# Performance work log

Measured on AMD Instinct MI355X. Metric: run time of the kernel, lower is better.

The kernel has to match this reference:

```python
import jax, jax.numpy as jnp
import numpy as np

N, E = 100000, 1600000
IN, T, H, C = 56, 16, 4, 16
HID, OUT = 64, 64
NEG_SLOPE = 0.2   # PyG GATConv default negative_slope
LN_EPS = 1e-5


def setup_inputs() -> dict:
    key = jax.random.key(0)
    k = jax.random.split(key, 12)
    g = lambda kk, shape: jax.random.normal(kk, shape, jnp.float32) * 0.1
    return {
        "x": jax.random.normal(k[0], (N, IN), jnp.float32),
        "temporal_features": jax.random.normal(k[1], (N, 1), jnp.float32),
        "edge_index": jax.random.randint(k[2], (2, E), 0, N, dtype=jnp.int32),
        "Wt": g(k[3], (1, T)), "bt": jnp.zeros((T,), jnp.float32),
        "W1": g(k[4], (IN + T, H * C)), "a_src1": g(k[5], (H, C)), "a_dst1": g(k[6], (H, C)),
        "b1": jnp.zeros((HID,), jnp.float32),
        "g1": jnp.ones((HID,), jnp.float32), "beta1": jnp.zeros((HID,), jnp.float32),
        "W2": g(k[7], (HID, H * C)), "a_src2": g(k[8], (H, C)), "a_dst2": g(k[9], (H, C)),
        "b2": jnp.zeros((OUT,), jnp.float32),
        "g2": jnp.ones((OUT,), jnp.float32), "beta2": jnp.zeros((OUT,), jnp.float32),
        "Wp1": g(k[10], (OUT, HID)), "bp1": jnp.zeros((HID,), jnp.float32),
        "Wp2": g(k[11], (HID, OUT)), "bp2": jnp.zeros((OUT,), jnp.float32),
    }


def _layer_norm(x, gamma, beta):
    mu = jnp.mean(x, -1, keepdims=True)
    var = jnp.var(x, -1, keepdims=True)
    return (x - mu) * jax.lax.rsqrt(var + LN_EPS) * gamma + beta


def _gat(x, src, dst, W, a_src, a_dst, bias, n):
    # linear transform per head (lin has no bias in PyG GATConv)
    h = (x @ W).reshape(n, H, C)                       # [N,H,C]
    s = jnp.einsum('nhc,hc->nh', h, a_src)             # att_src . h, per node
    d = jnp.einsum('nhc,hc->nh', h, a_dst)             # att_dst . h, per node
    e = jax.nn.leaky_relu(s[src] + d[dst], NEG_SLOPE)  # [Etot,H] per-edge logits
    # segment softmax over destination node (PyG softmax with +1e-16 denom)
    m = jax.ops.segment_max(e, dst, num_segments=n)
    e = jnp.exp(e - m[dst])
    z = jax.ops.segment_sum(e, dst, num_segments=n)
    alpha = e / (z[dst] + 1e-16)
    out = jax.ops.segment_sum(alpha[:, :, None] * h[src], dst, num_segments=n)
    return out.reshape(n, H * C) + bias


def reference(x, temporal_features, edge_index, Wt, bt, W1, a_src1, a_dst1, b1, g1, beta1,
              W2, a_src2, a_dst2, b2, g2, beta2, Wp1, bp1, Wp2, bp2):
    n = x.shape[0]
    t = jax.nn.relu(temporal_features @ Wt + bt)       # temporal encoder (dropout=identity, eval)
    xc = jnp.concatenate([x, t], axis=1)               # [N, 72]
    # add self-loops (PyG GATConv default add_self_loops=True)
    loop = jnp.arange(n, dtype=edge_index.dtype)
    src = jnp.concatenate([edge_index[0], loop])
    dst = jnp.concatenate([edge_index[1], loop])
    x1 = jax.nn.relu(_layer_norm(_gat(xc, src, dst, W1, a_src1, a_dst1, b1, n), g1, beta1))
    x2 = jax.nn.relu(_layer_norm(_gat(x1, src, dst, W2, a_src2, a_dst2, b2, n), g2, beta2))
    ge = jnp.mean(x2, axis=0)                          # batch=None -> global mean over nodes
    ge = jax.nn.relu(ge @ Wp1 + bp1) @ Wp2 + bp2       # global_pool MLP, then squeeze(0)
    return x2, ge
```

## Files before the change

### kernel.cpp

```cpp
#include <hip/hip_runtime.h>
#include <hip/hip_bf16.h>

#define NN    100000
#define EE    1600000
#define INF   56
#define TFEAT 16
#define K1    72

#define BUCKET_BITS 10
#define BUCKET_NODES (1 << BUCKET_BITS)
#define NB ((NN + BUCKET_NODES - 1) >> BUCKET_BITS)
#define BUCKET_CAP 20480
#define S1_EDGES 1024

__device__ __forceinline__ void fatomic_add(float* p, float v) {
    __hip_atomic_fetch_add(p, v, __ATOMIC_RELAXED, __HIP_MEMORY_SCOPE_AGENT);
}

__device__ __forceinline__ float lrelu(float v) { return v > 0.f ? v : 0.2f * v; }
__device__ __forceinline__ float bf2f(__hip_bfloat16 b) { return __bfloat162float(b); }
__device__ __forceinline__ float bfu2f(unsigned short u) {
    return __uint_as_float((unsigned)u << 16);
}
__device__ __forceinline__ unsigned short f2bfu(float f) {
    __hip_bfloat16 b = __float2bfloat16(f);
    return *reinterpret_cast<unsigned short*>(&b);
}

template <int K, bool TEMPORAL, bool IN_BF16>
__global__ void __launch_bounds__(256) feat_kernel(
    const void* __restrict__ xin_, const float* __restrict__ temp,
    const float* __restrict__ Wt, const float* __restrict__ bt,
    const float* __restrict__ W, const float* __restrict__ asrc,
    const float* __restrict__ adst,
    __hip_bfloat16* __restrict__ h, float* __restrict__ s, float* __restrict__ d)
{
    constexpr int NPB = 64;
    constexpr int WROW = 76;
    __shared__ float4 Wl4[K * 16];
    __shared__ __align__(16) float xc[NPB * WROW];
    const int tid = threadIdx.x;
    const int n0 = blockIdx.x * NPB;

    for (int i = tid; i < K * 16; i += 256)
        Wl4[i] = *(const float4*)&W[(i >> 4) * 64 + (i & 15) * 4];

    if (TEMPORAL) {
        const float* xin = (const float*)xin_;
        for (int i = tid; i < NPB * INF; i += 256) {
            int n = i / INF, k = i - n * INF;
            int gn = n0 + n;
            xc[n * WROW + k] = (gn < NN) ? xin[gn * INF + k] : 0.f;
        }
        for (int i = tid; i < NPB * TFEAT; i += 256) {
            int n = i >> 4, j = i & 15;
            int gn = n0 + n;
            float tv = (gn < NN) ? temp[gn] * Wt[j] + bt[j] : 0.f;
            xc[n * WROW + INF + j] = tv > 0.f ? tv : 0.f;
        }
    } else {
        const ushort4* xv4 = (const ushort4*)xin_;
        for (int i = tid; i < NPB * 16; i += 256) {
            int n = i >> 4, q = i & 15;
            int gn = n0 + n;
            float4 f = {0.f, 0.f, 0.f, 0.f};
            if (gn < NN) {
                ushort4 u = xv4[gn * 16 + q];
                f.x = bfu2f(u.x); f.y = bfu2f(u.y); f.z = bfu2f(u.z); f.w = bfu2f(u.w);
            }
            *(float4*)&xc[n * WROW + q * 4] = f;
        }
    }
    __syncthreads();

    const int w = tid >> 6, lane = tid & 63;
    const int li = lane & 15, gg = lane >> 4;
    const int nb = w * 16 + gg * 4;

    float4 a0 = {0,0,0,0}, a1 = {0,0,0,0}, a2 = {0,0,0,0}, a3 = {0,0,0,0};
    const float4* xr0 = (const float4*)&xc[(nb + 0) * WROW];
    const float4* xr1 = (const float4*)&xc[(nb + 1) * WROW];
    const float4* xr2 = (const float4*)&xc[(nb + 2) * WROW];
    const float4* xr3 = (const float4*)&xc[(nb + 3) * WROW];

#define FMA4(A, XV) \
    A.x += XV.x * w0.x + XV.y * w1.x + XV.z * w2.x + XV.w * w3.x; \
    A.y += XV.x * w0.y + XV.y * w1.y + XV.z * w2.y + XV.w * w3.y; \
    A.z += XV.x * w0.z + XV.y * w1.z + XV.z * w2.z + XV.w * w3.z; \
    A.w += XV.x * w0.w + XV.y * w1.w + XV.z * w2.w + XV.w * w3.w;

#pragma unroll
    for (int k4 = 0; k4 < K / 4; k4++) {
        float4 w0 = Wl4[(4 * k4 + 0) * 16 + li];
        float4 w1 = Wl4[(4 * k4 + 1) * 16 + li];
        float4 w2 = Wl4[(4 * k4 + 2) * 16 + li];
        float4 w3 = Wl4[(4 * k4 + 3) * 16 + li];
        float4 x0 = xr0[k4], x1 = xr1[k4], x2 = xr2[k4], x3 = xr3[k4];
        FMA4(a0, x0) FMA4(a1, x1) FMA4(a2, x2) FMA4(a3, x3)
    }
#undef FMA4

    const int head = li >> 2;
    const float4 as4 = *(const float4*)&asrc[li * 4];
    const float4 ad4 = *(const float4*)&adst[li * 4];
    float vs[4], vd[4];
    float4* ap[4] = {&a0, &a1, &a2, &a3};
#pragma unroll
    for (int j = 0; j < 4; j++) {
        float4 a = *ap[j];
        vs[j] = a.x * as4.x + a.y * as4.y + a.z * as4.z + a.w * as4.w;
        vd[j] = a.x * ad4.x + a.y * ad4.y + a.z * ad4.z + a.w * ad4.w;
        vs[j] += __shfl_xor(vs[j], 1); vs[j] += __shfl_xor(vs[j], 2);
        vd[j] += __shfl_xor(vd[j], 1); vd[j] += __shfl_xor(vd[j], 2);
    }

    ushort4* hv4 = (ushort4*)h;
#pragma unroll
    for (int j = 0; j < 4; j++) {
        int gn = n0 + nb + j;
        if (gn < NN) {
            float4 a = *ap[j];
            ushort4 st = { f2bfu(a.x), f2bfu(a.y), f2bfu(a.z), f2bfu(a.w) };
            hv4[gn * 16 + li] = st;
            if ((li & 3) == 0) { s[gn * 4 + head] = vs[j]; d[gn * 4 + head] = vd[j]; }
        }
    }
}

__global__ void __launch_bounds__(256) csr_s1_kernel(
    const int* __restrict__ esrc, const int* __restrict__ edst,
    int* __restrict__ bucketCnt, int* __restrict__ ebuf)
{
    __shared__ int hist[NB];
    __shared__ int base[NB];
    __shared__ int loff[NB];
    const int tid = threadIdx.x;
    const int e0 = blockIdx.x * S1_EDGES;

    for (int i = tid; i < NB; i += 256) { hist[i] = 0; loff[i] = 0; }
    __syncthreads();

    int val[4], bk[4];
#pragma unroll
    for (int t = 0; t < 4; t++) {
        int e = e0 + t * 256 + tid;
        if (e < EE) {
            int sn = esrc[e], dn = edst[e];
            int b = dn >> BUCKET_BITS;
            bk[t] = b;
            val[t] = ((dn & (BUCKET_NODES - 1)) << 17) | sn;
            atomicAdd(&hist[b], 1);
        } else bk[t] = -1;
    }
    __syncthreads();
    for (int i = tid; i < NB; i += 256)
        base[i] = hist[i] ? atomicAdd(&bucketCnt[i], hist[i]) : 0;
    __syncthreads();
#pragma unroll
    for (int t = 0; t < 4; t++) {
        if (bk[t] >= 0) {
            int pos = atomicAdd(&loff[bk[t]], 1);
            ebuf[bk[t] * BUCKET_CAP + base[bk[t]] + pos] = val[t];
        }
    }
}

__global__ void __launch_bounds__(256) csr_s2_kernel(
    const int* __restrict__ bucketCnt, const int* __restrict__ ebuf,
    int* __restrict__ deg, int* __restrict__ rowptr, int* __restrict__ csr_src)
{
    __shared__ int hist2[BUCKET_NODES];
    __shared__ int wsum[4];
    __shared__ int partial[256];
    const int b = blockIdx.x;
    const int tid = threadIdx.x;
    const int cnt = bucketCnt[b];
    const int nb0 = b << BUCKET_BITS;
    const int nnodes = min(BUCKET_NODES, NN - nb0);
    const int* seg = ebuf + b * BUCKET_CAP;

    partial[tid] = (tid < b) ? bucketCnt[tid] : 0;
    __syncthreads();
    for (int o = 128; o; o >>= 1) {
        if (tid < o) partial[tid] += partial[tid + o];
        __syncthreads();
    }
    const int cbase = partial[0];
    __syncthreads();

    for (int i = tid; i < BUCKET_NODES; i += 256) hist2[i] = 0;
    __syncthreads();
    for (int e = tid; e < cnt; e += 256) atomicAdd(&hist2[seg[e] >> 17], 1);
    __syncthreads();

    const int i0 = tid * 4;
    int h0 = hist2[i0], h1 = hist2[i0 + 1], h2 = hist2[i0 + 2], h3 = hist2[i0 + 3];
    int local = h0 + h1 + h2 + h3;
    int lane = tid & 63, wid = tid >> 6;
    int inc = local;
    for (int o = 1; o < 64; o <<= 1) {
        int u = __shfl_up(inc, o);
        if (lane >= o) inc += u;
    }
    if (lane == 63) wsum[wid] = inc;
    __syncthreads();
    int wbase = 0;
    for (int w = 0; w < wid; w++) wbase += wsum[w];
    int ebase = wbase + inc - local;
    __syncthreads();

    if (i0 < nnodes)     { deg[nb0 + i0]     = h0; rowptr[nb0 + i0]     = cbase + ebase; }
    if (i0 + 1 < nnodes) { deg[nb0 + i0 + 1] = h1; rowptr[nb0 + i0 + 1] = cbase + ebase + h0; }
    if (i0 + 2 < nnodes) { deg[nb0 + i0 + 2] = h2; rowptr[nb0 + i0 + 2] = cbase + ebase + h0 + h1; }
    if (i0 + 3 < nnodes) { deg[nb0 + i0 + 3] = h3; rowptr[nb0 + i0 + 3] = cbase + ebase + h0 + h1 + h2; }
    hist2[i0]     = ebase;
    hist2[i0 + 1] = ebase + h0;
    hist2[i0 + 2] = ebase + h0 + h1;
    hist2[i0 + 3] = ebase + h0 + h1 + h2;
    __syncthreads();

    for (int e = tid; e < cnt; e += 256) {
        int v = seg[e];
        int pos = atomicAdd(&hist2[v >> 17], 1);
        csr_src[cbase + pos] = v & 0x1FFFF;
    }
}

template <bool OUT_BF16>
__global__ void __launch_bounds__(256) agg_ln_kernel(
    const int* __restrict__ csr_src, const int* __restrict__ rowptr, const int* __restrict__ deg,
    const float* __restrict__ s, const float* __restrict__ d, const __hip_bfloat16* __restrict__ h,
    const float* __restrict__ bias, const float* __restrict__ gamma, const float* __restrict__ beta,
    void* __restrict__ out_)
{
    const int tid = threadIdx.x;
    const int wid = tid >> 6, lane = tid & 63;
    const int g = lane >> 4;
    const int li = lane & 15;
    const int head = li >> 2;
    const int c0 = li * 4;
    const int n = blockIdx.x * 16 + wid * 4 + g;

    const ushort4* hv4 = (const ushort4*)h;

    const float dv = d[n * 4 + head];
    float a0, a1, a2, a3, z;
    {
        float w = __expf(lrelu(s[n * 4 + head] + dv));
        ushort4 hv = hv4[n * 16 + li];
        a0 = w * bfu2f(hv.x); a1 = w * bfu2f(hv.y);
        a2 = w * bfu2f(hv.z); a3 = w * bfu2f(hv.w);
        z = w;
    }
    int j = rowptr[n];
    const int jend = j + deg[n];
    for (; j + 2 <= jend; j += 2) {
        int s0 = csr_src[j], s1 = csr_src[j + 1];
        float w0 = __expf(lrelu(s[s0 * 4 + head] + dv));
        float w1 = __expf(lrelu(s[s1 * 4 + head] + dv));
        ushort4 h0 = hv4[s0 * 16 + li];
        ushort4 h1 = hv4[s1 * 16 + li];
        a0 += w0 * bfu2f(h0.x) + w1 * bfu2f(h1.x);
        a1 += w0 * bfu2f(h0.y) + w1 * bfu2f(h1.y);
        a2 += w0 * bfu2f(h0.z) + w1 * bfu2f(h1.z);
        a3 += w0 * bfu2f(h0.w) + w1 * bfu2f(h1.w);
        z += w0 + w1;
    }
    if (j < jend) {
        int s0 = csr_src[j];
        float w0 = __expf(lrelu(s[s0 * 4 + head] + dv));
        ushort4 h0 = hv4[s0 * 16 + li];
        a0 += w0 * bfu2f(h0.x); a1 += w0 * bfu2f(h0.y);
        a2 += w0 * bfu2f(h0.z); a3 += w0 * bfu2f(h0.w);
        z += w0;
    }

    const float rz = 1.f / (z + 1e-16f);
    const float4 bv = *(const float4*)&bias[c0];
    float v0 = a0 * rz + bv.x, v1 = a1 * rz + bv.y;
    float v2 = a2 * rz + bv.z, v3 = a3 * rz + bv.w;

    float sum = (v0 + v1) + (v2 + v3);
    float sq  = (v0 * v0 + v1 * v1) + (v2 * v2 + v3 * v3);
#pragma unroll
    for (int o = 8; o; o >>= 1) { sum += __shfl_xor(sum, o); sq += __shfl_xor(sq, o); }
    float mu = sum * (1.f / 64.f);
    float var = sq * (1.f / 64.f) - mu * mu;
    float rs = rsqrtf(var + 1e-5f);
    const float4 gv = *(const float4*)&gamma[c0];
    const float4 bev = *(const float4*)&beta[c0];
    float y0 = (v0 - mu) * rs * gv.x + bev.x; y0 = y0 > 0.f ? y0 : 0.f;
    float y1 = (v1 - mu) * rs * gv.y + bev.y; y1 = y1 > 0.f ? y1 : 0.f;
    float y2 = (v2 - mu) * rs * gv.z + bev.z; y2 = y2 > 0.f ? y2 : 0.f;
    float y3 = (v3 - mu) * rs * gv.w + bev.w; y3 = y3 > 0.f ? y3 : 0.f;

    if (OUT_BF16) {
        ushort4 st = { f2bfu(y0), f2bfu(y1), f2bfu(y2), f2bfu(y3) };
        ((ushort4*)out_)[n * 16 + li] = st;
    } else {
        float4 st = { y0, y1, y2, y3 };
        ((float4*)out_)[n * 16 + li] = st;
    }
}

__global__ void __launch_bounds__(256) mean_kernel(const float* __restrict__ xin, float* __restrict__ meanacc) {
    __shared__ float sd[256];
    const int wid = threadIdx.x >> 6, c = threadIdx.x & 63;
    float csum = 0.f;
    for (int grp = blockIdx.x; grp < NN / 4; grp += 512) {
        int n = grp * 4 + wid;
        csum += xin[n * 64 + c];
    }
    sd[threadIdx.x] = csum;
    __syncthreads();
    if (threadIdx.x < 64) {
        fatomic_add(&meanacc[threadIdx.x],
                    sd[threadIdx.x] + sd[64 + threadIdx.x] + sd[128 + threadIdx.x] + sd[192 + threadIdx.x]);
    }
}

__global__ void __launch_bounds__(64) mlp_kernel(
    const float* __restrict__ meanacc,
    const float* __restrict__ Wp1, const float* __restrict__ bp1,
    const float* __restrict__ Wp2, const float* __restrict__ bp2,
    float* __restrict__ out)
{
    __shared__ float mean[64], hid[64];
    int t = threadIdx.x;
    mean[t] = meanacc[t] * (1.f / (float)NN);
    __syncthreads();
    float acc = bp1[t];
#pragma unroll
    for (int i = 0; i < 64; i++) acc += mean[i] * Wp1[i * 64 + t];
    hid[t] = acc > 0.f ? acc : 0.f;
    __syncthreads();
    float o = bp2[t];
#pragma unroll
    for (int i = 0; i < 64; i++) o += hid[i] * Wp2[i * 64 + t];
    out[NN * 64 + t] = o;
}

extern "C" void kernel_launch(void* const* d_in, const int* in_sizes, int n_in,
                              void* d_out, int out_size, void* d_ws, size_t ws_size,
                              hipStream_t stream) {
    const float* x    = (const float*)d_in[0];
    const float* temp = (const float*)d_in[1];
    const int*   ei   = (const int*)d_in[2];
    const float* Wt   = (const float*)d_in[3];
    const float* bt   = (const float*)d_in[4];
    const float* W1   = (const float*)d_in[5];
    const float* as1  = (const float*)d_in[6];
    const float* ad1  = (const float*)d_in[7];
    const float* b1   = (const float*)d_in[8];
    const float* g1   = (const float*)d_in[9];
    const float* be1  = (const float*)d_in[10];
    const float* W2   = (const float*)d_in[11];
    const float* as2  = (const float*)d_in[12];
    const float* ad2  = (const float*)d_in[13];
    const float* b2   = (const float*)d_in[14];
    const float* g2   = (const float*)d_in[15];
    const float* be2  = (const float*)d_in[16];
    const float* Wp1  = (const float*)d_in[17];
    const float* bp1  = (const float*)d_in[18];
    const float* Wp2  = (const float*)d_in[19];
    const float* bp2  = (const float*)d_in[20];

    float* out = (float*)d_out;

    char* w = (char*)d_ws;
    __hip_bfloat16* hb   = (__hip_bfloat16*)w;   w += (size_t)NN * 64 * 2;
    __hip_bfloat16* x1b  = (__hip_bfloat16*)w;   w += (size_t)NN * 64 * 2;
    float* sbuf    = (float*)w;                  w += (size_t)NN * 4 * 4;
    float* dbuf    = (float*)w;                  w += (size_t)NN * 4 * 4;
    float* meanacc = (float*)w;                  w += 256;
    int* bucketCnt = (int*)w;                    w += 512;
    int* deg       = (int*)w;                    w += (size_t)NN * 4;
    int* rowptr    = (int*)w;                    w += (size_t)NN * 4;
    int* csr_src   = (int*)w;                    w += (size_t)EE * 4;
    int* ebuf      = (int*)w;                    w += (size_t)NB * BUCKET_CAP * 4;

    const int* esrc = ei;
    const int* edst = ei + EE;

    hipMemsetAsync(bucketCnt, 0, 512, stream);
    hipMemsetAsync(meanacc, 0, 256, stream);

    csr_s1_kernel<<<(EE + S1_EDGES - 1) / S1_EDGES, 256, 0, stream>>>(esrc, edst, bucketCnt, ebuf);
    csr_s2_kernel<<<NB, 256, 0, stream>>>(bucketCnt, ebuf, deg, rowptr, csr_src);

    const int fgrid = (NN + 63) / 64;

    feat_kernel<K1, true, false><<<fgrid, 256, 0, stream>>>(x, temp, Wt, bt, W1, as1, ad1, hb, sbuf, dbuf);
    agg_ln_kernel<true><<<NN / 16, 256, 0, stream>>>(csr_src, rowptr, deg, sbuf, dbuf, hb, b1, g1, be1, x1b);

    feat_kernel<64, false, true><<<fgrid, 256, 0, stream>>>(x1b, nullptr, nullptr, nullptr, W2, as2, ad2, hb, sbuf, dbuf);
    agg_ln_kernel<false><<<NN / 16, 256, 0, stream>>>(csr_src, rowptr, deg, sbuf, dbuf, hb, b2, g2, be2, out);

    mean_kernel<<<512, 256, 0, stream>>>(out, meanacc);
    mlp_kernel<<<1, 64, 0, stream>>>(meanacc, Wp1, bp1, Wp2, bp2, out);
}
```

Baseline: 369.4 us.

## Degree-sort nodes, widen aggregation lanes, fold exp scaling, fuse global mean

```diff
diff --git a/kernel.cpp b/kernel.cpp
--- a/kernel.cpp
+++ b/kernel.cpp
@@ -12,13 +12,12 @@
 #define NB ((NN + BUCKET_NODES - 1) >> BUCKET_BITS)
 #define BUCKET_CAP 20480
 #define S1_EDGES 1024
+#define LOG2E 1.44269504f
 
 __device__ __forceinline__ void fatomic_add(float* p, float v) {
     __hip_atomic_fetch_add(p, v, __ATOMIC_RELAXED, __HIP_MEMORY_SCOPE_AGENT);
 }
 
-__device__ __forceinline__ float lrelu(float v) { return v > 0.f ? v : 0.2f * v; }
-__device__ __forceinline__ float bf2f(__hip_bfloat16 b) { return __bfloat162float(b); }
 __device__ __forceinline__ float bfu2f(unsigned short u) {
     return __uint_as_float((unsigned)u << 16);
 }
@@ -26,6 +25,9 @@
     __hip_bfloat16 b = __float2bfloat16(f);
     return *reinterpret_cast<unsigned short*>(&b);
 }
+__device__ __forceinline__ float blo(unsigned u) { return __uint_as_float(u << 16); }
+__device__ __forceinline__ float bhi(unsigned u) { return __uint_as_float(u & 0xFFFF0000u); }
+__device__ __forceinline__ float ew(float t) { return exp2f(fmaxf(t, 0.2f * t)); }
 
 template <int K, bool TEMPORAL, bool IN_BF16>
 __global__ void __launch_bounds__(256) feat_kernel(
@@ -122,7 +124,10 @@
             float4 a = *ap[j];
             ushort4 st = { f2bfu(a.x), f2bfu(a.y), f2bfu(a.z), f2bfu(a.w) };
             hv4[gn * 16 + li] = st;
-            if ((li & 3) == 0) { s[gn * 4 + head] = vs[j]; d[gn * 4 + head] = vd[j]; }
+            if ((li & 3) == 0) {
+                s[gn * 4 + head] = vs[j] * LOG2E;
+                d[gn * 4 + head] = vd[j] * LOG2E;
+            }
         }
     }
 }
@@ -167,11 +172,14 @@
 
 __global__ void __launch_bounds__(256) csr_s2_kernel(
     const int* __restrict__ bucketCnt, const int* __restrict__ ebuf,
-    int* __restrict__ deg, int* __restrict__ rowptr, int* __restrict__ csr_src)
+    int* __restrict__ deg, int* __restrict__ rowptr, int* __restrict__ csr_src,
+    int* __restrict__ perm)
 {
     __shared__ int hist2[BUCKET_NODES];
     __shared__ int wsum[4];
     __shared__ int partial[256];
+    __shared__ int dhist[64];
+    __shared__ int dcur[64];
     const int b = blockIdx.x;
     const int tid = threadIdx.x;
     const int cnt = bucketCnt[b];
@@ -224,110 +232,165 @@
         int pos = atomicAdd(&hist2[v >> 17], 1);
         csr_src[cbase + pos] = v & 0x1FFFF;
     }
+
+    if (tid < 64) { dhist[tid] = 0; }
+    __syncthreads();
+    int dkey[4] = { -1, -1, -1, -1 };
+    int dv_[4] = { h0, h1, h2, h3 };
+#pragma unroll
+    for (int jj = 0; jj < 4; jj++) {
+        if (i0 + jj < nnodes) {
+            dkey[jj] = min(dv_[jj], 63);
+            atomicAdd(&dhist[dkey[jj]], 1);
+        }
+    }
+    __syncthreads();
+    if (tid < 64) {
+        int v = dhist[tid];
+        int ic = v;
+        for (int o = 1; o < 64; o <<= 1) {
+            int u = __shfl_up(ic, o);
+            if (tid >= o) ic += u;
+        }
+        dcur[tid] = ic - v;
+    }
+    __syncthreads();
+#pragma unroll
+    for (int jj = 0; jj < 4; jj++) {
+        if (dkey[jj] >= 0) {
+            int pos = atomicAdd(&dcur[dkey[jj]], 1);
+            perm[nb0 + pos] = nb0 + i0 + jj;
+        }
+    }
 }
 
 template <bool OUT_BF16>
 __global__ void __launch_bounds__(256) agg_ln_kernel(
+    const int* __restrict__ perm,
     const int* __restrict__ csr_src, const int* __restrict__ rowptr, const int* __restrict__ deg,
     const float* __restrict__ s, const float* __restrict__ d, const __hip_bfloat16* __restrict__ h,
     const float* __restrict__ bias, const float* __restrict__ gamma, const float* __restrict__ beta,
-    void* __restrict__ out_)
+    void* __restrict__ out_, float* __restrict__ meanslots)
 {
+    __shared__ float sd[32 * 65];
     const int tid = threadIdx.x;
     const int wid = tid >> 6, lane = tid & 63;
-    const int g = lane >> 4;
-    const int li = lane & 15;
-    const int head = li >> 2;
-    const int c0 = li * 4;
-    const int n = blockIdx.x * 16 + wid * 4 + g;
-
-    const ushort4* hv4 = (const ushort4*)h;
-
-    const float dv = d[n * 4 + head];
-    float a0, a1, a2, a3, z;
+    const int g = lane >> 3;
+    const int li = lane & 7;
+    const int head = li >> 1;
+    const int n = blockIdx.x * 32 + wid * 8 + g;
+    const int p = perm[n];
+
+    const uint4* hv4 = (const uint4*)h;
+
+    const float dv = d[p * 4 + head];
+    float a0, a1, a2, a3, a4, a5, a6, a7, z;
     {
-        float w = __expf(lrelu(s[n * 4 + head] + dv));
-        ushort4 hv = hv4[n * 16 + li];
-        a0 = w * bfu2f(hv.x); a1 = w * bfu2f(hv.y);
-        a2 = w * bfu2f(hv.z); a3 = w * bfu2f(hv.w);
+        float w = ew(s[p * 4 + head] + dv);
+        uint4 u = hv4[p * 8 + li];
+        a0 = w * blo(u.x); a1 = w * bhi(u.x);
+        a2 = w * blo(u.y); a3 = w * bhi(u.y);
+        a4 = w * blo(u.z); a5 = w * bhi(u.z);
+        a6 = w * blo(u.w); a7 = w * bhi(u.w);
         z = w;
     }
-    int j = rowptr[n];
-    const int jend = j + deg[n];
+    int j = rowptr[p];
+    const int jend = j + deg[p];
     for (; j + 2 <= jend; j += 2) {
         int s0 = csr_src[j], s1 = csr_src[j + 1];
-        float w0 = __expf(lrelu(s[s0 * 4 + head] + dv));
-        float w1 = __expf(lrelu(s[s1 * 4 + head] + dv));
-        ushort4 h0 = hv4[s0 * 16 + li];
-        ushort4 h1 = hv4[s1 * 16 + li];
-        a0 += w0 * bfu2f(h0.x) + w1 * bfu2f(h1.x);
-        a1 += w0 * bfu2f(h0.y) + w1 * bfu2f(h1.y);
-        a2 += w0 * bfu2f(h0.z) + w1 * bfu2f(h1.z);
-        a3 += w0 * bfu2f(h0.w) + w1 * bfu2f(h1.w);
+        float w0 = ew(s[s0 * 4 + head] + dv);
+        float w1 = ew(s[s1 * 4 + head] + dv);
+        uint4 u0 = hv4[s0 * 8 + li];
+        uint4 u1 = hv4[s1 * 8 + li];
+        a0 += w0 * blo(u0.x) + w1 * blo(u1.x);
+        a1 += w0 * bhi(u0.x) + w1 * bhi(u1.x);
+        a2 += w0 * blo(u0.y) + w1 * blo(u1.y);
+        a3 += w0 * bhi(u0.y) + w1 * bhi(u1.y);
+        a4 += w0 * blo(u0.z) + w1 * blo(u1.z);
+        a5 += w0 * bhi(u0.z) + w1 * bhi(u1.z);
+        a6 += w0 * blo(u0.w) + w1 * blo(u1.w);
+        a7 += w0 * bhi(u0.w) + w1 * bhi(u1.w);
         z += w0 + w1;
     }
     if (j < jend) {
         int s0 = csr_src[j];
-        float w0 = __expf(lrelu(s[s0 * 4 + head] + dv));
-        ushort4 h0 = hv4[s0 * 16 + li];
-        a0 += w0 * bfu2f(h0.x); a1 += w0 * bfu2f(h0.y);
-        a2 += w0 * bfu2f(h0.z); a3 += w0 * bfu2f(h0.w);
+        float w0 = ew(s[s0 * 4 + head] + dv);
+        uint4 u0 = hv4[s0 * 8 + li];
+        a0 += w0 * blo(u0.x); a1 += w0 * bhi(u0.x);
+        a2 += w0 * blo(u0.y); a3 += w0 * bhi(u0.y);
+        a4 += w0 * blo(u0.z); a5 += w0 * bhi(u0.z);
+        a6 += w0 * blo(u0.w); a7 += w0 * bhi(u0.w);
         z += w0;
     }
 
     const float rz = 1.f / (z + 1e-16f);
-    const float4 bv = *(const float4*)&bias[c0];
-    float v0 = a0 * rz + bv.x, v1 = a1 * rz + bv.y;
-    float v2 = a2 * rz + bv.z, v3 = a3 * rz + bv.w;
-
-    float sum = (v0 + v1) + (v2 + v3);
-    float sq  = (v0 * v0 + v1 * v1) + (v2 * v2 + v3 * v3);
-#pragma unroll
-    for (int o = 8; o; o >>= 1) { sum += __shfl_xor(sum, o); sq += __shfl_xor(sq, o); }
+    const int c0 = li * 8;
+    const float4 bv0 = *(const float4*)&bias[c0];
+    const float4 bv1 = *(const float4*)&bias[c0 + 4];
+    float v0 = a0 * rz + bv0.x, v1 = a1 * rz + bv0.y;
+    float v2 = a2 * rz + bv0.z, v3 = a3 * rz + bv0.w;
+    float v4 = a4 * rz + bv1.x, v5 = a5 * rz + bv1.y;
+    float v6 = a6 * rz + bv1.z, v7 = a7 * rz + bv1.w;
+
+    float sum = ((v0 + v1) + (v2 + v3)) + ((v4 + v5) + (v6 + v7));
+    float sq  = ((v0 * v0 + v1 * v1) + (v2 * v2 + v3 * v3)) +
+                ((v4 * v4 + v5 * v5) + (v6 * v6 + v7 * v7));
+#pragma unroll
+    for (int o = 4; o; o >>= 1) { sum += __shfl_xor(sum, o); sq += __shfl_xor(sq, o); }
     float mu = sum * (1.f / 64.f);
     float var = sq * (1.f / 64.f) - mu * mu;
     float rs = rsqrtf(var + 1e-5f);
-    const float4 gv = *(const float4*)&gamma[c0];
-    const float4 bev = *(const float4*)&beta[c0];
-    float y0 = (v0 - mu) * rs * gv.x + bev.x; y0 = y0 > 0.f ? y0 : 0.f;
-    float y1 = (v1 - mu) * rs * gv.y + bev.y; y1 = y1 > 0.f ? y1 : 0.f;
-    float y2 = (v2 - mu) * rs * gv.z + bev.z; y2 = y2 > 0.f ? y2 : 0.f;
-    float y3 = (v3 - mu) * rs * gv.w + bev.w; y3 = y3 > 0.f ? y3 : 0.f;
+    const float4 gv0 = *(const float4*)&gamma[c0];
+    const float4 gv1 = *(const float4*)&gamma[c0 + 4];
+    const float4 be0 = *(const float4*)&beta[c0];
+    const float4 be1 = *(const float4*)&beta[c0 + 4];
+    float y0 = (v0 - mu) * rs * gv0.x + be0.x; y0 = y0 > 0.f ? y0 : 0.f;
+    float y1 = (v1 - mu) * rs * gv0.y + be0.y; y1 = y1 > 0.f ? y1 : 0.f;
+    float y2 = (v2 - mu) * rs * gv0.z + be0.z; y2 = y2 > 0.f ? y2 : 0.f;
+    float y3 = (v3 - mu) * rs * gv0.w + be0.w; y3 = y3 > 0.f ? y3 : 0.f;
+    float y4 = (v4 - mu) * rs * gv1.x + be1.x; y4 = y4 > 0.f ? y4 : 0.f;
+    float y5 = (v5 - mu) * rs * gv1.y + be1.y; y5 = y5 > 0.f ? y5 : 0.f;
+    float y6 = (v6 - mu) * rs * gv1.z + be1.z; y6 = y6 > 0.f ? y6 : 0.f;
+    float y7 = (v7 - mu) * rs * gv1.w + be1.w; y7 = y7 > 0.f ? y7 : 0.f;
 
     if (OUT_BF16) {
-        ushort4 st = { f2bfu(y0), f2bfu(y1), f2bfu(y2), f2bfu(y3) };
-        ((ushort4*)out_)[n * 16 + li] = st;
+        uint4 st;
+        st.x = (unsigned)f2bfu(y0) | ((unsigned)f2bfu(y1) << 16);
+        st.y = (unsigned)f2bfu(y2) | ((unsigned)f2bfu(y3) << 16);
+        st.z = (unsigned)f2bfu(y4) | ((unsigned)f2bfu(y5) << 16);
+        st.w = (unsigned)f2bfu(y6) | ((unsigned)f2bfu(y7) << 16);
+        ((uint4*)out_)[p * 8 + li] = st;
     } else {
-        float4 st = { y0, y1, y2, y3 };
-        ((float4*)out_)[n * 16 + li] = st;
-    }
-}
-
-__global__ void __launch_bounds__(256) mean_kernel(const float* __restrict__ xin, float* __restrict__ meanacc) {
-    __shared__ float sd[256];
-    const int wid = threadIdx.x >> 6, c = threadIdx.x & 63;
-    float csum = 0.f;
-    for (int grp = blockIdx.x; grp < NN / 4; grp += 512) {
-        int n = grp * 4 + wid;
-        csum += xin[n * 64 + c];
-    }
-    sd[threadIdx.x] = csum;
-    __syncthreads();
-    if (threadIdx.x < 64) {
-        fatomic_add(&meanacc[threadIdx.x],
-                    sd[threadIdx.x] + sd[64 + threadIdx.x] + sd[128 + threadIdx.x] + sd[192 + threadIdx.x]);
+        float4 st0 = { y0, y1, y2, y3 };
+        float4 st1 = { y4, y5, y6, y7 };
+        ((float4*)out_)[p * 16 + li * 2] = st0;
+        ((float4*)out_)[p * 16 + li * 2 + 1] = st1;
+        const int nloc = wid * 8 + g;
+        float* row = &sd[nloc * 65 + c0];
+        row[0] = y0; row[1] = y1; row[2] = y2; row[3] = y3;
+        row[4] = y4; row[5] = y5; row[6] = y6; row[7] = y7;
+        __syncthreads();
+        if (tid < 64) {
+            float psum = 0.f;
+#pragma unroll
+            for (int m = 0; m < 32; m++) psum += sd[m * 65 + tid];
+            fatomic_add(&meanslots[(blockIdx.x & 63) * 64 + tid], psum);
+        }
     }
 }
 
 __global__ void __launch_bounds__(64) mlp_kernel(
-    const float* __restrict__ meanacc,
+    const float* __restrict__ meanslots,
     const float* __restrict__ Wp1, const float* __restrict__ bp1,
     const float* __restrict__ Wp2, const float* __restrict__ bp2,
     float* __restrict__ out)
 {
     __shared__ float mean[64], hid[64];
     int t = threadIdx.x;
-    mean[t] = meanacc[t] * (1.f / (float)NN);
+    float accm = 0.f;
+#pragma unroll
+    for (int sIdx = 0; sIdx < 64; sIdx++) accm += meanslots[sIdx * 64 + t];
+    mean[t] = accm * (1.f / (float)NN);
     __syncthreads();
     float acc = bp1[t];
 #pragma unroll
@@ -372,30 +435,32 @@
     __hip_bfloat16* x1b  = (__hip_bfloat16*)w;   w += (size_t)NN * 64 * 2;
     float* sbuf    = (float*)w;                  w += (size_t)NN * 4 * 4;
     float* dbuf    = (float*)w;                  w += (size_t)NN * 4 * 4;
-    float* meanacc = (float*)w;                  w += 256;
     int* bucketCnt = (int*)w;                    w += 512;
+    float* meanslots = (float*)w;                w += 64 * 64 * 4;
     int* deg       = (int*)w;                    w += (size_t)NN * 4;
     int* rowptr    = (int*)w;                    w += (size_t)NN * 4;
+    int* perm      = (int*)w;                    w += (size_t)NN * 4;
     int* csr_src   = (int*)w;                    w += (size_t)EE * 4;
     int* ebuf      = (int*)w;                    w += (size_t)NB * BUCKET_CAP * 4;
 
     const int* esrc = ei;
     const int* edst = ei + EE;
 
-    hipMemsetAsync(bucketCnt, 0, 512, stream);
-    hipMemsetAsync(meanacc, 0, 256, stream);
+    hipMemsetAsync(bucketCnt, 0, 512 + 64 * 64 * 4, stream);
 
     csr_s1_kernel<<<(EE + S1_EDGES - 1) / S1_EDGES, 256, 0, stream>>>(esrc, edst, bucketCnt, ebuf);
-    csr_s2_kernel<<<NB, 256, 0, stream>>>(bucketCnt, ebuf, deg, rowptr, csr_src);
+    csr_s2_kernel<<<NB, 256, 0, stream>>>(bucketCnt, ebuf, deg, rowptr, csr_src, perm);
 
     const int fgrid = (NN + 63) / 64;
+    const int agrid = NN / 32;
 
     feat_kernel<K1, true, false><<<fgrid, 256, 0, stream>>>(x, temp, Wt, bt, W1, as1, ad1, hb, sbuf, dbuf);
-    agg_ln_kernel<true><<<NN / 16, 256, 0, stream>>>(csr_src, rowptr, deg, sbuf, dbuf, hb, b1, g1, be1, x1b);
+    agg_ln_kernel<true><<<agrid, 256, 0, stream>>>(perm, csr_src, rowptr, deg, sbuf, dbuf, hb,
+                                                   b1, g1, be1, x1b, meanslots);
 
     feat_kernel<64, false, true><<<fgrid, 256, 0, stream>>>(x1b, nullptr, nullptr, nullptr, W2, as2, ad2, hb, sbuf, dbuf);
-    agg_ln_kernel<false><<<NN / 16, 256, 0, stream>>>(csr_src, rowptr, deg, sbuf, dbuf, hb, b2, g2, be2, out);
-
-    mean_kernel<<<512, 256, 0, stream>>>(out, meanacc);
-    mlp_kernel<<<1, 64, 0, stream>>>(meanacc, Wp1, bp1, Wp2, bp2, out);
-}
+    agg_ln_kernel<false><<<agrid, 256, 0, stream>>>(perm, csr_src, rowptr, deg, sbuf, dbuf, hb,
+                                                    b2, g2, be2, out, meanslots);
+
+    mlp_kernel<<<1, 64, 0, stream>>>(meanslots, Wp1, bp1, Wp2, bp2, out);
+}
```

After: 357.1 us. 3.3% less time.
